# Optimization experiments

Measured on AMD Instinct MI355X. Metric: run time of the kernel, lower is better.

## Reference

```python
import jax, jax.numpy as jnp
import numpy as np

B, T, C_IN, H, W = 4096, 256, 16, 1, 1
HID, NCLS = 64, 10


def setup_inputs() -> dict:
    key = jax.random.key(0)
    ks = jax.random.split(key, 8)
    s = 0.1
    x = jax.random.normal(ks[0], (B, T, C_IN, H, W), dtype=jnp.float32)
    # ConvLSTM cell: 1x1 conv over concat([x_t, h]) -> 4*HID gate channels
    W_lstm = jax.random.normal(ks[1], (4 * HID, C_IN + HID), dtype=jnp.float32) * s
    b_lstm = jnp.zeros((4 * HID,), dtype=jnp.float32)
    W_class = jax.random.normal(ks[2], (NCLS, HID), dtype=jnp.float32) * s
    b_class = jnp.zeros((NCLS,), dtype=jnp.float32)
    W_dec = jax.random.normal(ks[3], (1, HID), dtype=jnp.float32) * s
    b_dec = jnp.zeros((1,), dtype=jnp.float32)
    return {"x": x, "W_lstm": W_lstm, "b_lstm": b_lstm,
            "W_class": W_class, "b_class": b_class,
            "W_dec": W_dec, "b_dec": b_dec}


def _conv1x1(z, Wm, bv):
    # 1x1 conv == channel contraction; z: [B,C,H,W], Wm: [O,C]
    return jnp.einsum('bchw,oc->bohw', z, Wm) + bv[None, :, None, None]


def reference(x, W_lstm, b_lstm, W_class, b_class, W_dec, b_dec):
    Bn, Tn, Cn, Hn, Wn = x.shape
    hid = W_class.shape[1]
    h0 = jnp.zeros((Bn, hid, Hn, Wn), dtype=x.dtype)
    c0 = jnp.zeros((Bn, hid, Hn, Wn), dtype=x.dtype)
    pnd0 = jnp.ones((Bn, Hn, Wn), dtype=x.dtype)  # proba_not_decided_yet

    def step(carry, xt):
        h, c, pnd = carry
        comb = jnp.concatenate([xt, h], axis=1)
        gates = _conv1x1(comb, W_lstm, b_lstm)
        i, f, o, g = jnp.split(gates, 4, axis=1)
        c_next = jax.nn.sigmoid(f) * c + jax.nn.sigmoid(i) * jnp.tanh(g)
        h_next = jax.nn.sigmoid(o) * jnp.tanh(c_next)
        dec = jax.nn.sigmoid(_conv1x1(h_next, W_dec, b_dec))[:, 0]  # [B,H,W]
        logp = jax.nn.log_softmax(_conv1x1(h_next, W_class, b_class), axis=1)
        pnd_next = pnd * (1.0 - dec)
        return (h_next, c_next, pnd_next), (logp, dec, pnd)

    xt_seq = jnp.moveaxis(x, 1, 0)  # [T,B,C,H,W]
    _, (logps, decs, pnds) = jax.lax.scan(step, (h0, c0, pnd0), xt_seq)
    logps = jnp.moveaxis(logps, 0, 1)  # [B,T,NCLS,H,W]
    decs = jnp.moveaxis(decs, 0, 1)    # [B,T,H,W]
    pnds = jnp.moveaxis(pnds, 0, 1)    # pnd BEFORE step t
    is_last = (jnp.arange(Tn) == Tn - 1)[None, :, None, None]
    # Pt = dec_t * pnd_t for t < T-1 ; Pt = pnd_{T-1} at the last step
    Pts = jnp.where(is_last, pnds, decs * pnds)
    return logps, Pts
```

## Files before the change

### kernel.cpp

```cpp
#include <hip/hip_runtime.h>
#include <hip/hip_bf16.h>

#define Bsz  4096
#define Tn   256
#define CIN  16
#define NCLS 10
#define MB   16

typedef __attribute__((ext_vector_type(8))) short short8;
typedef __attribute__((ext_vector_type(4))) float f32x4;

#if __has_builtin(__builtin_amdgcn_exp2f)
#define EXP2F(x) __builtin_amdgcn_exp2f(x)
#else
#define EXP2F(x) exp2f(x)
#endif
#define RCPF(x) __builtin_amdgcn_rcpf(x)

#define LOG2E 1.442695041f

#define BARRIER_LDS() do {                                     \
    asm volatile("s_waitcnt lgkmcnt(0)" ::: "memory");         \
    __builtin_amdgcn_s_barrier();                              \
} while (0)

__device__ inline ushort f2bf(float f) {
    union { float f; unsigned u; } x; x.f = f;
    return (ushort)((x.u + 0x7FFF + ((x.u >> 16) & 1)) >> 16);
}

__global__ __launch_bounds__(512, 2) void dualrnn_fused(
    const float* __restrict__ x,  const float* __restrict__ Wl, const float* __restrict__ bl,
    const float* __restrict__ Wc, const float* __restrict__ bc,
    const float* __restrict__ Wd, const float* __restrict__ bd,
    float* __restrict__ out)
{
    __shared__ alignas(16) ushort comb[2][16][104];
    const int tid  = threadIdx.x;
    const int wave = tid >> 6;
    const int lane = tid & 63;
    const int col  = lane & 15;
    const int grp  = lane >> 4;
    const int b0   = blockIdx.x * MB;
    const bool gatew = (wave < 4);

    for (int i = tid; i < 2 * 16 * 104; i += 512) ((ushort*)comb)[i] = 0;

    short8 wf[4][3]; f32x4 biasv[4];
    short8 wcd[2];   f32x4 bcdv;
    if (gatew) {
#pragma unroll
        for (int g = 0; g < 4; ++g) {
            const float sc = (g == 3) ? 2.f * LOG2E : -LOG2E;
            const int R = g * 64 + wave * 16 + col;
            const float bv = bl[R] * sc;
            biasv[g] = (f32x4){bv, bv, bv, bv};
#pragma unroll
            for (int kt = 0; kt < 3; ++kt)
#pragma unroll
                for (int i = 0; i < 8; ++i) {
                    const int k = kt * 32 + grp * 8 + i;
                    wf[g][kt][i] = (short)f2bf(k < 80 ? Wl[R * 80 + k] * sc : 0.f);
                }
        }
    } else {
#pragma unroll
        for (int kt = 0; kt < 2; ++kt)
#pragma unroll
            for (int i = 0; i < 8; ++i) {
                const int k = kt * 32 + grp * 8 + i;
                float v = 0.f;
                if (col < 10)       v = Wc[col * 64 + k];
                else if (col == 10) v = Wd[k] * -LOG2E;
                wcd[kt][i] = (short)f2bf(v);
            }
        const float bv = (col < 10) ? bc[col] : ((col == 10) ? bd[0] * -LOG2E : 0.f);
        bcdv = (f32x4){bv, bv, bv, bv};
    }

    __syncthreads();

    if (tid < 256) {
        const int r = tid >> 4, ch = tid & 15;
        comb[0][r][ch] = f2bf(x[((size_t)(b0 + r) * Tn) * CIN + ch]);
    }
    __syncthreads();

    float cst[4] = {0, 0, 0, 0};
    float pnd = 1.f;

    const int hw  = wave & 3;
    const int row = grp * 4 + hw;
    float* lp_p = out + ((size_t)(b0 + row) * Tn) * NCLS + col;
    float* pt_p = out + (size_t)Bsz * Tn * NCLS + (size_t)(b0 + row) * Tn;
    const int t2 = hw * 64 + lane;
    const int xr = t2 >> 4, xc = t2 & 15;
    float xva = 0.f;
    const float* xp = x + ((size_t)(b0 + xr) * Tn + 2) * CIN + xc;
    if (!gatew) xva = x[((size_t)(b0 + xr) * Tn + 1) * CIN + xc];

    for (int t = 0; t < Tn; ++t) {
        const ushort (*rdb)[104] = comb[t & 1];
        ushort (*wrb)[104] = comb[(t + 1) & 1];
        if (gatew) {
            const short8 a0 = *(const short8*)&rdb[col][ 0 + grp * 8];
            const short8 a1 = *(const short8*)&rdb[col][32 + grp * 8];
            const short8 a2 = *(const short8*)&rdb[col][64 + grp * 8];
            f32x4 acc[4];
#pragma unroll
            for (int g = 0; g < 4; ++g) {
                f32x4 z = biasv[g];
                z = __builtin_amdgcn_mfma_f32_16x16x32_bf16(a0, wf[g][0], z, 0, 0, 0);
                z = __builtin_amdgcn_mfma_f32_16x16x32_bf16(a1, wf[g][1], z, 0, 0, 0);
                z = __builtin_amdgcn_mfma_f32_16x16x32_bf16(a2, wf[g][2], z, 0, 0, 0);
                acc[g] = z;
            }
            const int hc = 16 + wave * 16 + col;
#pragma unroll
            for (int j = 0; j < 4; ++j) {
                const float ei = EXP2F(acc[0][j]);
                const float ef = EXP2F(acc[1][j]);
                const float eo = EXP2F(acc[2][j]);
                const float eg = EXP2F(acc[3][j]);
                const float A  = 1.f + ei, Bv = 1.f + ef;
                const float G1 = eg + 1.f, G2 = eg - 1.f, O = 1.f + eo;
                const float t0  = A * G1;
                const float num = cst[j] * t0 + G2 * Bv;
                const float den = Bv * t0;
                const float cn  = num * RCPF(den);
                cst[j] = cn;
                const float e2 = EXP2F(2.f * LOG2E * cn);
                const float h  = (e2 - 1.f) * RCPF((e2 + 1.f) * O);
                wrb[grp * 4 + j][hc] = f2bf(h);
            }
        } else {
            float xvn = 0.f;
            if (t + 2 < Tn) xvn = *xp;
            xp += CIN;
            const short8 ha0 = *(const short8*)&rdb[col][16 + grp * 8];
            const short8 ha1 = *(const short8*)&rdb[col][48 + grp * 8];
            f32x4 cz = bcdv;
            cz = __builtin_amdgcn_mfma_f32_16x16x32_bf16(ha0, wcd[0], cz, 0, 0, 0);
            cz = __builtin_amdgcn_mfma_f32_16x16x32_bf16(ha1, wcd[1], cz, 0, 0, 0);
            if (t + 1 < Tn) wrb[xr][xc] = f2bf(xva);
            xva = xvn;
            if (t > 0) {
                float v = (hw & 1) ? ((hw & 2) ? cz[3] : cz[1])
                                   : ((hw & 2) ? cz[2] : cz[0]);
                float s = (col < 10) ? EXP2F(v * LOG2E) : 0.f;
                s += __int_as_float(__builtin_amdgcn_ds_swizzle(__float_as_int(s), 0x041F));
                s += __int_as_float(__builtin_amdgcn_ds_swizzle(__float_as_int(s), 0x081F));
                s += __int_as_float(__builtin_amdgcn_ds_swizzle(__float_as_int(s), 0x101F));
                s += __int_as_float(__builtin_amdgcn_ds_swizzle(__float_as_int(s), 0x201F));
                const float lse = __logf(s);
                if (col < 10) {
                    lp_p[0] = v - lse;
                } else if (col == 10) {
                    const float d = RCPF(1.f + EXP2F(v));
                    pt_p[0] = d * pnd;
                    pnd *= (1.f - d);
                }
                lp_p += NCLS;
                pt_p += 1;
            }
        }
        BARRIER_LDS();
    }

    if (!gatew) {
        const ushort (*rdb)[104] = comb[Tn & 1];
        const short8 ha0 = *(const short8*)&rdb[col][16 + grp * 8];
        const short8 ha1 = *(const short8*)&rdb[col][48 + grp * 8];
        f32x4 cz = bcdv;
        cz = __builtin_amdgcn_mfma_f32_16x16x32_bf16(ha0, wcd[0], cz, 0, 0, 0);
        cz = __builtin_amdgcn_mfma_f32_16x16x32_bf16(ha1, wcd[1], cz, 0, 0, 0);
        float v = (hw & 1) ? ((hw & 2) ? cz[3] : cz[1])
                           : ((hw & 2) ? cz[2] : cz[0]);
        float s = (col < 10) ? EXP2F(v * LOG2E) : 0.f;
        s += __int_as_float(__builtin_amdgcn_ds_swizzle(__float_as_int(s), 0x041F));
        s += __int_as_float(__builtin_amdgcn_ds_swizzle(__float_as_int(s), 0x081F));
        s += __int_as_float(__builtin_amdgcn_ds_swizzle(__float_as_int(s), 0x101F));
        s += __int_as_float(__builtin_amdgcn_ds_swizzle(__float_as_int(s), 0x201F));
        const float lse = __logf(s);
        if (col < 10)       lp_p[0] = v - lse;
        else if (col == 10) pt_p[0] = pnd;
    }
}

extern "C" void kernel_launch(void* const* d_in, const int* in_sizes, int n_in,
                              void* d_out, int out_size, void* d_ws, size_t ws_size,
                              hipStream_t stream) {
    const float* x  = (const float*)d_in[0];
    const float* Wl = (const float*)d_in[1];
    const float* bl = (const float*)d_in[2];
    const float* Wc = (const float*)d_in[3];
    const float* bc = (const float*)d_in[4];
    const float* Wd = (const float*)d_in[5];
    const float* bd = (const float*)d_in[6];
    float* out = (float*)d_out;

    hipLaunchKernelGGL(dualrnn_fused, dim3(Bsz / MB), dim3(512), 0, stream,
                       x, Wl, bl, Wc, bc, Wd, bd, out);
}
```

Measured before the change: 148.7 us.

## Split LSTM cell activations between gate and head waves via LDS

Gate waves write half of their gate pre-activations to shared memory, and the otherwise idle classifier/decision waves compute the cell update for those rows. This halves the serial transcendental work on the gate waves' critical path. The cost is an extra LDS round-trip and an additional block barrier per timestep. Classifier weights are also pre-scaled by log2(e) so one exp2 serves both the softmax sum and the decision sigmoid.

```diff
diff --git a/kernel.cpp b/kernel.cpp
--- a/kernel.cpp
+++ b/kernel.cpp
@@ -18,6 +18,7 @@
 #define RCPF(x) __builtin_amdgcn_rcpf(x)
 
 #define LOG2E 1.442695041f
+#define LN2   0.6931471806f
 
 #define BARRIER_LDS() do {                                     \
     asm volatile("s_waitcnt lgkmcnt(0)" ::: "memory");         \
@@ -27,6 +28,22 @@
 __device__ inline ushort f2bf(float f) {
     union { float f; unsigned u; } x; x.f = f;
     return (ushort)((x.u + 0x7FFF + ((x.u >> 16) & 1)) >> 16);
+}
+
+__device__ inline float cell_act(float& c, float ai, float af, float ao, float ag) {
+    const float ei = EXP2F(ai);
+    const float ef = EXP2F(af);
+    const float eo = EXP2F(ao);
+    const float eg = EXP2F(ag);
+    const float A  = 1.f + ei, Bv = 1.f + ef;
+    const float G1 = eg + 1.f, G2 = eg - 1.f, O = 1.f + eo;
+    const float t0  = A * G1;
+    const float num = c * t0 + G2 * Bv;
+    const float den = Bv * t0;
+    const float cn  = num * RCPF(den);
+    c = cn;
+    const float e2 = EXP2F(2.f * LOG2E * cn);
+    return (e2 - 1.f) * RCPF((e2 + 1.f) * O);
 }
 
 __global__ __launch_bounds__(512, 2) void dualrnn_fused(
@@ -36,6 +53,7 @@
     float* __restrict__ out)
 {
     __shared__ alignas(16) ushort comb[2][16][104];
+    __shared__ alignas(16) float accT[4][2][64][4];
     const int tid  = threadIdx.x;
     const int wave = tid >> 6;
     const int lane = tid & 63;
@@ -43,6 +61,7 @@
     const int grp  = lane >> 4;
     const int b0   = blockIdx.x * MB;
     const bool gatew = (wave < 4);
+    const int slot = grp * 16 + col;
 
     for (int i = tid; i < 2 * 16 * 104; i += 512) ((ushort*)comb)[i] = 0;
 
@@ -70,11 +89,12 @@
             for (int i = 0; i < 8; ++i) {
                 const int k = kt * 32 + grp * 8 + i;
                 float v = 0.f;
-                if (col < 10)       v = Wc[col * 64 + k];
+                if (col < 10)       v = Wc[col * 64 + k] * LOG2E;
                 else if (col == 10) v = Wd[k] * -LOG2E;
                 wcd[kt][i] = (short)f2bf(v);
             }
-        const float bv = (col < 10) ? bc[col] : ((col == 10) ? bd[0] * -LOG2E : 0.f);
+        const float bv = (col < 10) ? bc[col] * LOG2E
+                       : ((col == 10) ? bd[0] * -LOG2E : 0.f);
         bcdv = (f32x4){bv, bv, bv, bv};
     }
 
@@ -86,7 +106,7 @@
     }
     __syncthreads();
 
-    float cst[4] = {0, 0, 0, 0};
+    float cst[2] = {0, 0};
     float pnd = 1.f;
 
     const int hw  = wave & 3;
@@ -103,6 +123,7 @@
         const ushort (*rdb)[104] = comb[t & 1];
         ushort (*wrb)[104] = comb[(t + 1) & 1];
         if (gatew) {
+            const int ub = wave;
             const short8 a0 = *(const short8*)&rdb[col][ 0 + grp * 8];
             const short8 a1 = *(const short8*)&rdb[col][32 + grp * 8];
             const short8 a2 = *(const short8*)&rdb[col][64 + grp * 8];
@@ -115,23 +136,18 @@
                 z = __builtin_amdgcn_mfma_f32_16x16x32_bf16(a2, wf[g][2], z, 0, 0, 0);
                 acc[g] = z;
             }
-            const int hc = 16 + wave * 16 + col;
-#pragma unroll
-            for (int j = 0; j < 4; ++j) {
-                const float ei = EXP2F(acc[0][j]);
-                const float ef = EXP2F(acc[1][j]);
-                const float eo = EXP2F(acc[2][j]);
-                const float eg = EXP2F(acc[3][j]);
-                const float A  = 1.f + ei, Bv = 1.f + ef;
-                const float G1 = eg + 1.f, G2 = eg - 1.f, O = 1.f + eo;
-                const float t0  = A * G1;
-                const float num = cst[j] * t0 + G2 * Bv;
-                const float den = Bv * t0;
-                const float cn  = num * RCPF(den);
-                cst[j] = cn;
-                const float e2 = EXP2F(2.f * LOG2E * cn);
-                const float h  = (e2 - 1.f) * RCPF((e2 + 1.f) * O);
-                wrb[grp * 4 + j][hc] = f2bf(h);
+#pragma unroll
+            for (int jj = 0; jj < 2; ++jj) {
+                f32x4 tv = {acc[0][jj + 2], acc[1][jj + 2], acc[2][jj + 2], acc[3][jj + 2]};
+                *(f32x4*)&accT[ub][jj][slot][0] = tv;
+            }
+            BARRIER_LDS();
+            const int hc = 16 + ub * 16 + col;
+#pragma unroll
+            for (int jj = 0; jj < 2; ++jj) {
+                const float h = cell_act(cst[jj], acc[0][jj], acc[1][jj],
+                                         acc[2][jj], acc[3][jj]);
+                wrb[grp * 4 + jj][hc] = f2bf(h);
             }
         } else {
             float xvn = 0.f;
@@ -147,21 +163,30 @@
             if (t > 0) {
                 float v = (hw & 1) ? ((hw & 2) ? cz[3] : cz[1])
                                    : ((hw & 2) ? cz[2] : cz[0]);
-                float s = (col < 10) ? EXP2F(v * LOG2E) : 0.f;
+                const float e = EXP2F(v);
+                float s = (col < 10) ? e : 0.f;
                 s += __int_as_float(__builtin_amdgcn_ds_swizzle(__float_as_int(s), 0x041F));
                 s += __int_as_float(__builtin_amdgcn_ds_swizzle(__float_as_int(s), 0x081F));
                 s += __int_as_float(__builtin_amdgcn_ds_swizzle(__float_as_int(s), 0x101F));
                 s += __int_as_float(__builtin_amdgcn_ds_swizzle(__float_as_int(s), 0x201F));
                 const float lse = __logf(s);
                 if (col < 10) {
-                    lp_p[0] = v - lse;
+                    lp_p[0] = v * LN2 - lse;
                 } else if (col == 10) {
-                    const float d = RCPF(1.f + EXP2F(v));
+                    const float d = RCPF(1.f + e);
                     pt_p[0] = d * pnd;
                     pnd *= (1.f - d);
                 }
                 lp_p += NCLS;
                 pt_p += 1;
+            }
+            BARRIER_LDS();
+            const int hc = 16 + hw * 16 + col;
+#pragma unroll
+            for (int jj = 0; jj < 2; ++jj) {
+                const f32x4 tv = *(const f32x4*)&accT[hw][jj][slot][0];
+                const float h = cell_act(cst[jj], tv[0], tv[1], tv[2], tv[3]);
+                wrb[grp * 4 + 2 + jj][hc] = f2bf(h);
             }
         }
         BARRIER_LDS();
@@ -176,13 +201,14 @@
         cz = __builtin_amdgcn_mfma_f32_16x16x32_bf16(ha1, wcd[1], cz, 0, 0, 0);
         float v = (hw & 1) ? ((hw & 2) ? cz[3] : cz[1])
                            : ((hw & 2) ? cz[2] : cz[0]);
-        float s = (col < 10) ? EXP2F(v * LOG2E) : 0.f;
+        const float e = EXP2F(v);
+        float s = (col < 10) ? e : 0.f;
         s += __int_as_float(__builtin_amdgcn_ds_swizzle(__float_as_int(s), 0x041F));
         s += __int_as_float(__builtin_amdgcn_ds_swizzle(__float_as_int(s), 0x081F));
         s += __int_as_float(__builtin_amdgcn_ds_swizzle(__float_as_int(s), 0x101F));
         s += __int_as_float(__builtin_amdgcn_ds_swizzle(__float_as_int(s), 0x201F));
         const float lse = __logf(s);
-        if (col < 10)       lp_p[0] = v - lse;
+        if (col < 10)       lp_p[0] = v * LN2 - lse;
         else if (col == 10) pt_p[0] = pnd;
     }
 }
```

New measurement: 189.6 us. 1.28x slower.
